# Optimization experiments

Measured on AMD Instinct MI355X. Metric: run time of the kernel, lower is better.

## Reference

```python
import jax, jax.numpy as jnp
import numpy as np

B, C, H, W = 2, 256, 64, 64
N_HEAD = 4
GROUPS = 32
EPS = 1e-5


def setup_inputs() -> dict:
    key = jax.random.key(0)
    ks = jax.random.split(key, 6)
    x = jax.random.normal(ks[0], (B, C, H, W), dtype=jnp.float32)
    # GroupNorm affine (perturbed from torch default 1/0 so grads are nontrivial)
    gn_scale = 1.0 + 0.02 * jax.random.normal(ks[1], (C,), dtype=jnp.float32)
    gn_bias = 0.02 * jax.random.normal(ks[2], (C,), dtype=jnp.float32)
    # 1x1 convs == pointwise matmuls: qkv (bias=False), out (bias=True)
    w_qkv = 0.02 * jax.random.normal(ks[3], (3 * C, C), dtype=jnp.float32)
    w_out = 0.02 * jax.random.normal(ks[4], (C, C), dtype=jnp.float32)
    b_out = 0.02 * jax.random.normal(ks[5], (C,), dtype=jnp.float32)
    return {"x": x, "gn_scale": gn_scale, "gn_bias": gn_bias,
            "w_qkv": w_qkv, "w_out": w_out, "b_out": b_out}


def _group_norm(x, scale, bias):
    b, c, h, w = x.shape
    xr = x.reshape(b, GROUPS, c // GROUPS, h, w)
    mean = jnp.mean(xr, axis=(2, 3, 4), keepdims=True)
    var = jnp.var(xr, axis=(2, 3, 4), keepdims=True)
    xr = (xr - mean) * jax.lax.rsqrt(var + EPS)
    x = xr.reshape(b, c, h, w)
    return x * scale[None, :, None, None] + bias[None, :, None, None]


def reference(x, gn_scale, gn_bias, w_qkv, w_out, b_out):
    b, c, h, w = x.shape
    head_dim = c // N_HEAD
    n = h * w
    norm = _group_norm(x, gn_scale, gn_bias)
    # 1x1 conv -> pointwise channel matmul; flatten spatial to n = h*w tokens
    qkv = jnp.einsum('oc,bcn->bon', w_qkv, norm.reshape(b, c, n))
    qkv = qkv.reshape(b, N_HEAD, 3 * head_dim, n)
    q, k, v = jnp.split(qkv, 3, axis=2)  # each [b, n_head, head_dim, n]
    # NOTE: original scales by sqrt(channel), not sqrt(head_dim)
    attn = jnp.einsum('bndq,bndk->bnqk', q, k) / jnp.sqrt(jnp.float32(c))
    attn = jax.nn.softmax(attn, axis=-1)  # [b, n_head, n, n]
    out = jnp.einsum('bnqk,bndk->bndq', attn, v)  # [b, n_head, head_dim, n]
    out = out.reshape(b, c, n)
    out = jnp.einsum('oc,bcn->bon', w_out, out) + b_out[None, :, None]
    return out.reshape(b, c, h, w) + x
```

## Files before the change

### kernel.cpp

```cpp
#include <hip/hip_runtime.h>
#include <hip/hip_bf16.h>

#define Bz 2
#define Cc 256
#define Nn 4096
#define NH 4
#define HD 64
#define NG 32
#define CPG 8
#define EPSv 1e-5f
#define NSPLIT 4
#define GNPART 4

typedef __bf16 bf16x8 __attribute__((ext_vector_type(8)));
typedef __bf16 bf16x4 __attribute__((ext_vector_type(4)));
typedef float f32x4 __attribute__((ext_vector_type(4)));
using bf16_t = __hip_bfloat16;

#define MFMA(a, b, c) __builtin_amdgcn_mfma_f32_16x16x32_bf16(a, b, c, 0, 0, 0)

#define GLOAD_LDS(g, l)                                                        \
  __builtin_amdgcn_global_load_lds(                                            \
      (const __attribute__((address_space(1))) void*)(g),                      \
      (__attribute__((address_space(3))) void*)(l), 16, 0, 0)

#define EXP2(x)                                                                \
  ({ float _r, _x = (x); asm("v_exp_f32 %0, %1" : "=v"(_r) : "v"(_x)); _r; })

__device__ __forceinline__ bf16x8 ldb8(const bf16_t* p) {
  return *reinterpret_cast<const bf16x8*>(p);
}

__global__ __launch_bounds__(256) void gn_reduce(const float* __restrict__ x,
                                                 float* __restrict__ stats4) {
  int bg = blockIdx.x;
  int part = blockIdx.y;
  const float4* p4 = reinterpret_cast<const float4*>(
      x + (size_t)bg * (CPG * Nn) + (size_t)part * (CPG * Nn / GNPART));
  float s = 0.f, ss = 0.f;
  for (int i = threadIdx.x; i < CPG * Nn / GNPART / 4; i += 256) {
    float4 v = p4[i];
    s += v.x + v.y + v.z + v.w;
    ss += v.x * v.x + v.y * v.y + v.z * v.z + v.w * v.w;
  }
#pragma unroll
  for (int off = 32; off > 0; off >>= 1) {
    s += __shfl_down(s, off);
    ss += __shfl_down(ss, off);
  }
  __shared__ float ps[4], pss[4];
  int wid = threadIdx.x >> 6;
  if ((threadIdx.x & 63) == 0) { ps[wid] = s; pss[wid] = ss; }
  __syncthreads();
  if (threadIdx.x == 0) {
    stats4[(bg * GNPART + part) * 2] = ps[0] + ps[1] + ps[2] + ps[3];
    stats4[(bg * GNPART + part) * 2 + 1] = pss[0] + pss[1] + pss[2] + pss[3];
  }
}

__global__ __launch_bounds__(256) void gn_apply(const float* __restrict__ x,
    const float* __restrict__ stats4, const float* __restrict__ sc,
    const float* __restrict__ bi, bf16_t* __restrict__ normt) {
  int b = blockIdx.z, c0 = blockIdx.y * 64, n0 = blockIdx.x * 64;
  __shared__ __align__(16) __bf16 t[64][72];
  int cx = threadIdx.x & 15, cy0 = threadIdx.x >> 4;
  const float inv = 1.f / (float)(CPG * Nn);
#pragma unroll
  for (int j = 0; j < 4; j++) {
    int c = c0 + cy0 + j * 16;
    int bg = b * NG + (c >> 3);
    float S = stats4[bg * 8] + stats4[bg * 8 + 2] + stats4[bg * 8 + 4] + stats4[bg * 8 + 6];
    float SS = stats4[bg * 8 + 1] + stats4[bg * 8 + 3] + stats4[bg * 8 + 5] + stats4[bg * 8 + 7];
    float mean = S * inv;
    float rstd = rsqrtf(SS * inv - mean * mean + EPSv);
    float a = rstd * sc[c];
    float bb = bi[c] - mean * a;
    float4 v = *reinterpret_cast<const float4*>(x + ((size_t)b * Cc + c) * Nn + n0 + cx * 4);
    bf16x4 w;
    w[0] = (__bf16)(v.x * a + bb); w[1] = (__bf16)(v.y * a + bb);
    w[2] = (__bf16)(v.z * a + bb); w[3] = (__bf16)(v.w * a + bb);
    *reinterpret_cast<bf16x4*>(&t[cy0 + j * 16][cx * 4]) = w;
  }
  __syncthreads();
  int ny = threadIdx.x >> 2, ch0 = threadIdx.x & 3;
#pragma unroll
  for (int j = 0; j < 2; j++) {
    int ch = ch0 + j * 4;
    bf16x8 o;
#pragma unroll
    for (int jj = 0; jj < 8; jj++) o[jj] = t[ch * 8 + jj][ny];
    *reinterpret_cast<bf16x8*>(normt + ((size_t)b * Nn + n0 + ny) * Cc + c0 + ch * 8) = o;
  }
}

__global__ __launch_bounds__(256) void conv_w(const float* __restrict__ wq,
    const float* __restrict__ wo, bf16_t* __restrict__ wqb,
    bf16_t* __restrict__ wob) {
  int i = blockIdx.x * 256 + threadIdx.x;
  if (i < 768 * Cc) wqb[i] = __float2bfloat16(wq[i]);
  if (i < Cc * Cc) wob[i] = __float2bfloat16(wo[i]);
}

__global__ __launch_bounds__(512) void qkv_gemm(const bf16_t* __restrict__ normt,
    const bf16_t* __restrict__ w, bf16_t* __restrict__ Qt,
    bf16_t* __restrict__ Kt, bf16_t* __restrict__ V) {
  int b = blockIdx.z;
  int h = blockIdx.y;
  int n0 = blockIdx.x * 128;
  int tid = threadIdx.x;
  int wid = tid >> 6, lane = tid & 63;
  int lr = lane & 15, lk = lane >> 4;

  __shared__ __align__(16) bf16_t wbuf[64 * 256];
  __shared__ __align__(16) __bf16 tt[128 * 80];

  const bf16_t* an = normt + ((size_t)b * Nn + n0 + wid * 16 + lr) * Cc + lk * 8;
  bf16x8 a[8];
#pragma unroll
  for (int kk = 0; kk < 8; kk++) a[kk] = ldb8(an + kk * 32);

#pragma unroll
  for (int part = 0; part < 3; part++) {
    int o0 = h * 192 + part * 64;
#pragma unroll
    for (int rnd = 0; rnd < 4; rnd++) {
      int u = rnd * 512 + tid;
      int row = u >> 5, cu = u & 31;
      int cus = (cu & 24) | ((cu & 7) ^ (row & 7));
      GLOAD_LDS(w + (size_t)(o0 + row) * Cc + cus * 8, &wbuf[u * 8]);
    }
    __syncthreads();
    f32x4 acc[4] = {};
#pragma unroll
    for (int kk = 0; kk < 8; kk++)
#pragma unroll
      for (int os = 0; os < 4; os++) {
        bf16x8 bb = ldb8(&wbuf[(os * 16 + lr) * Cc + (((kk * 4 + lk) ^ (lr & 7)) * 8)]);
        acc[os] = MFMA(a[kk], bb, acc[os]);
      }
#pragma unroll
    for (int os = 0; os < 4; os++)
#pragma unroll
      for (int r = 0; r < 4; r++)
        tt[(wid * 16 + lk * 4 + r) * 80 + os * 16 + lr] = (__bf16)acc[os][r];
    __syncthreads();
    if (part < 2) {
      bf16_t* dst = (part == 0 ? Qt : Kt) + (size_t)(b * NH + h) * Nn * HD + (size_t)n0 * HD;
      int n = tid >> 2, dch = (tid & 3) * 16;
      bf16x8 o1 = ldb8(reinterpret_cast<const bf16_t*>(&tt[n * 80 + dch]));
      bf16x8 o2 = ldb8(reinterpret_cast<const bf16_t*>(&tt[n * 80 + dch + 8]));
      *reinterpret_cast<bf16x8*>(dst + (size_t)n * HD + dch) = o1;
      *reinterpret_cast<bf16x8*>(dst + (size_t)n * HD + dch + 8) = o2;
    } else {
      bf16_t* dst = V + (size_t)(b * NH + h) * HD * Nn + n0;
      int d = tid >> 3, nch = (tid & 7) * 16;
      bf16x8 o1, o2;
#pragma unroll
      for (int j = 0; j < 8; j++) {
        o1[j] = tt[(nch + j) * 80 + d];
        o2[j] = tt[(nch + 8 + j) * 80 + d];
      }
      *reinterpret_cast<bf16x8*>(dst + (size_t)d * Nn + nch) = o1;
      *reinterpret_cast<bf16x8*>(dst + (size_t)d * Nn + nch + 8) = o2;
    }
  }
}

__global__ __launch_bounds__(256, 2) void attn_kern(const bf16_t* __restrict__ Qt,
    const bf16_t* __restrict__ Kt, const bf16_t* __restrict__ V,
    bf16_t* __restrict__ Opart, float* __restrict__ ml) {
  int z = blockIdx.z;
  int b = z & 1, sp = z >> 1;
  int h = blockIdx.y;
  int tid = threadIdx.x;
  int wid = tid >> 6, lane = tid & 63;
  int lr = lane & 15, lk = lane >> 4;
  int q0 = blockIdx.x * 256 + wid * 64;
  size_t bh = (size_t)(b * NH + h);
  const float lam = 0.0625f * 1.44269504088896f;

  const bf16_t* qp = Qt + (bh * Nn + q0 + lr) * HD + lk * 8;
  bf16x8 aqA0, aqA1, aqB0, aqB1, aqC0, aqC1, aqD0, aqD1, vone;
  {
    bf16x8 tA0 = ldb8(qp), tA1 = ldb8(qp + 32);
    bf16x8 tB0 = ldb8(qp + 16 * HD), tB1 = ldb8(qp + 16 * HD + 32);
    bf16x8 tC0 = ldb8(qp + 32 * HD), tC1 = ldb8(qp + 32 * HD + 32);
    bf16x8 tD0 = ldb8(qp + 48 * HD), tD1 = ldb8(qp + 48 * HD + 32);
#pragma unroll
    for (int j = 0; j < 8; j++) {
      aqA0[j] = (__bf16)((float)tA0[j] * lam);
      aqA1[j] = (__bf16)((float)tA1[j] * lam);
      aqB0[j] = (__bf16)((float)tB0[j] * lam);
      aqB1[j] = (__bf16)((float)tB1[j] * lam);
      aqC0[j] = (__bf16)((float)tC0[j] * lam);
      aqC1[j] = (__bf16)((float)tC1[j] * lam);
      aqD0[j] = (__bf16)((float)tD0[j] * lam);
      aqD1[j] = (__bf16)((float)tD1[j] * lam);
      vone[j] = (__bf16)1.0f;
    }
  }
  const bf16_t* kglob = Kt + bh * Nn * HD;
  const bf16_t* vglob = V + bh * HD * Nn;
  int kbeg = sp * (Nn / NSPLIT);

  __shared__ __align__(16) char lds[69632];

  int krow0 = ((wid & 1) * 64 + lane) >> 3;
  int kswz = ((lane & 7) ^ (krow0 & 7)) * 8;
  const bf16_t* ks0 = kglob + (size_t)(kbeg + krow0) * HD + kswz;
  const bf16_t* vs0 = vglob + (size_t)krow0 * Nn + kbeg + kswz;
  int kdst = (wid & 1) * 1024;

  int x0 = lr & 7;
  int aK = lr * 128 + ((lk ^ x0) * 16);
  int aK1 = aK ^ 64;
  int pwoA = 32768 + wid * 9216 + lr * 144 + lk * 8;
  int proA = 32768 + wid * 9216 + lr * 144 + lk * 16;
  int pwoB = pwoA + 2304, proB = proA + 2304;
  int pwoC = pwoA + 4608, proC = proA + 4608;
  int pwoD = pwoA + 6912, proD = proA + 6912;

  f32x4 accA[4] = {}, accB[4] = {}, accC[4] = {}, accD[4] = {};
  f32x4 l4A = {}, l4B = {}, l4C = {}, l4D = {};
  const int NT = (Nn / NSPLIT) / 64;

#define LD8(off) (*reinterpret_cast<const bf16x8*>(lds + (off)))

#define STAGE(buf, t)                                                          \
  do {                                                                         \
    if (wid < 2) {                                                             \
      GLOAD_LDS(ks0 + (size_t)(t) * 64 * HD, lds + (buf) * 8192 + kdst);       \
      GLOAD_LDS(ks0 + (size_t)(t) * 64 * HD + 16 * HD,                         \
                lds + (buf) * 8192 + kdst + 2048);                             \
      GLOAD_LDS(ks0 + (size_t)(t) * 64 * HD + 32 * HD,                         \
                lds + (buf) * 8192 + kdst + 4096);                             \
      GLOAD_LDS(ks0 + (size_t)(t) * 64 * HD + 48 * HD,                         \
                lds + (buf) * 8192 + kdst + 6144);                             \
    } else {                                                                   \
      GLOAD_LDS(vs0 + (size_t)(t) * 64, lds + 16384 + (buf) * 8192 + kdst);    \
      GLOAD_LDS(vs0 + (size_t)(t) * 64 + (size_t)16 * Nn,                      \
                lds + 16384 + (buf) * 8192 + kdst + 2048);                     \
      GLOAD_LDS(vs0 + (size_t)(t) * 64 + (size_t)32 * Nn,                      \
                lds + 16384 + (buf) * 8192 + kdst + 4096);                     \
      GLOAD_LDS(vs0 + (size_t)(t) * 64 + (size_t)48 * Nn,                      \
                lds + 16384 + (buf) * 8192 + kdst + 6144);                     \
    }                                                                          \
  } while (0)

#define QKM(m, OFF)                                                            \
  do {                                                                         \
    bf16x8 kf0 = LD8(aK + (OFF) + (m) * 2048);                                 \
    bf16x8 kf1 = LD8(aK1 + (OFF) + (m) * 2048);                                \
    sA##m = MFMA(kf0, aqA0, sA##m); sA##m = MFMA(kf1, aqA1, sA##m);            \
    sB##m = MFMA(kf0, aqB0, sB##m); sB##m = MFMA(kf1, aqB1, sB##m);            \
    sC##m = MFMA(kf0, aqC0, sC##m); sC##m = MFMA(kf1, aqC1, sC##m);            \
    sD##m = MFMA(kf0, aqD0, sD##m); sD##m = MFMA(kf1, aqD1, sD##m);            \
  } while (0)

#define PVM(m, OFF)                                                            \
  do {                                                                         \
    bf16x8 vf0 = LD8(aK + 16384 + (OFF) + (m) * 2048);                         \
    bf16x8 vf1 = LD8(aK1 + 16384 + (OFF) + (m) * 2048);                        \
    accA[m] = MFMA(vf0, paA0, accA[m]); accA[m] = MFMA(vf1, paA1, accA[m]);    \
    accB[m] = MFMA(vf0, paB0, accB[m]); accB[m] = MFMA(vf1, paB1, accB[m]);    \
    accC[m] = MFMA(vf0, paC0, accC[m]); accC[m] = MFMA(vf1, paC1, accC[m]);    \
    accD[m] = MFMA(vf0, paD0, accD[m]); accD[m] = MFMA(vf1, paD1, accD[m]);    \
  } while (0)

#define SMG(G)                                                                 \
  do {                                                                         \
    f32x4 p0, p1, p2, p3;                                                      \
    _Pragma("unroll") for (int r = 0; r < 4; r++) {                            \
      p0[r] = EXP2(s##G##0[r]); p1[r] = EXP2(s##G##1[r]);                      \
      p2[r] = EXP2(s##G##2[r]); p3[r] = EXP2(s##G##3[r]);                      \
    }                                                                          \
    bf16x4 w0, w1, w2, w3;                                                     \
    _Pragma("unroll") for (int r = 0; r < 4; r++) {                            \
      w0[r] = (__bf16)p0[r]; w1[r] = (__bf16)p1[r];                            \
      w2[r] = (__bf16)p2[r]; w3[r] = (__bf16)p3[r];                            \
    }                                                                          \
    *reinterpret_cast<bf16x4*>(lds + pwo##G) = w0;                             \
    *reinterpret_cast<bf16x4*>(lds + pwo##G + 32) = w1;                        \
    *reinterpret_cast<bf16x4*>(lds + pwo##G + 64) = w2;                        \
    *reinterpret_cast<bf16x4*>(lds + pwo##G + 96) = w3;                        \
  } while (0)

#define STEP(t, buf)                                                           \
  do {                                                                         \
    __syncthreads();                                                           \
    STAGE(buf ^ 1, (t) + 1);                                                   \
    f32x4 sA0 = {}, sA1 = {}, sA2 = {}, sA3 = {};                              \
    f32x4 sB0 = {}, sB1 = {}, sB2 = {}, sB3 = {};                              \
    f32x4 sC0 = {}, sC1 = {}, sC2 = {}, sC3 = {};                              \
    f32x4 sD0 = {}, sD1 = {}, sD2 = {}, sD3 = {};                              \
    __builtin_amdgcn_s_setprio(1);                                             \
    QKM(0, (buf) * 8192); QKM(1, (buf) * 8192);                                \
    QKM(2, (buf) * 8192); QKM(3, (buf) * 8192);                                \
    __builtin_amdgcn_s_setprio(0);                                             \
    SMG(A); SMG(B); SMG(C); SMG(D);                                            \
    bf16x8 paA0 = LD8(proA), paA1 = LD8(proA + 64);                            \
    bf16x8 paB0 = LD8(proB), paB1 = LD8(proB + 64);                            \
    bf16x8 paC0 = LD8(proC), paC1 = LD8(proC + 64);                            \
    bf16x8 paD0 = LD8(proD), paD1 = LD8(proD + 64);                            \
    __builtin_amdgcn_s_setprio(1);                                             \
    PVM(0, (buf) * 8192); PVM(1, (buf) * 8192);                                \
    PVM(2, (buf) * 8192); PVM(3, (buf) * 8192);                                \
    l4A = MFMA(vone, paA0, l4A); l4A = MFMA(vone, paA1, l4A);                  \
    l4B = MFMA(vone, paB0, l4B); l4B = MFMA(vone, paB1, l4B);                  \
    l4C = MFMA(vone, paC0, l4C); l4C = MFMA(vone, paC1, l4C);                  \
    l4D = MFMA(vone, paD0, l4D); l4D = MFMA(vone, paD1, l4D);                  \
    __builtin_amdgcn_s_setprio(0);                                             \
  } while (0)

  STAGE(0, 0);
  for (int t = 0; t < NT; t += 2) {
    STEP(t, 0);
    STEP(t + 1, 1);
  }
#undef STEP
#undef STAGE
#undef QKM
#undef PVM
#undef SMG
#undef LD8

  float invA = 1.f / l4A[0], invB = 1.f / l4B[0];
  float invC = 1.f / l4C[0], invD = 1.f / l4D[0];
  bf16_t* obA = Opart + (((size_t)z * NH + h) * Nn + q0 + lr) * HD + lk * 4;
  bf16_t* obB = obA + (size_t)16 * HD;
  bf16_t* obC = obA + (size_t)32 * HD;
  bf16_t* obD = obA + (size_t)48 * HD;
#pragma unroll
  for (int dt = 0; dt < 4; dt++) {
    bf16x4 vA, vB, vC, vD;
#pragma unroll
    for (int r = 0; r < 4; r++) {
      vA[r] = (__bf16)(accA[dt][r] * invA);
      vB[r] = (__bf16)(accB[dt][r] * invB);
      vC[r] = (__bf16)(accC[dt][r] * invC);
      vD[r] = (__bf16)(accD[dt][r] * invD);
    }
    *reinterpret_cast<bf16x4*>(obA + dt * 16) = vA;
    *reinterpret_cast<bf16x4*>(obB + dt * 16) = vB;
    *reinterpret_cast<bf16x4*>(obC + dt * 16) = vC;
    *reinterpret_cast<bf16x4*>(obD + dt * 16) = vD;
  }
  if (lk == 0) {
    size_t mb = ((size_t)z * NH + h) * Nn + q0 + lr;
    ml[mb] = l4A[0];
    ml[mb + 16] = l4B[0];
    ml[mb + 32] = l4C[0];
    ml[mb + 48] = l4D[0];
  }
}

__global__ __launch_bounds__(256) void attn_merge(const bf16_t* __restrict__ Opart,
    const float* __restrict__ ml, bf16_t* __restrict__ At) {
  int gid = blockIdx.x * 256 + threadIdx.x;
  int d0 = (gid & 7) * 8;
  int q = (gid >> 3) & (Nn - 1);
  int h = (gid >> 15) & (NH - 1);
  int b = gid >> 17;
  size_t zi[NSPLIT];
  float lv[NSPLIT];
  float L = 0.f;
#pragma unroll
  for (int s = 0; s < NSPLIT; s++) {
    zi[s] = ((size_t)(s * Bz + b) * NH + h) * Nn + q;
    lv[s] = ml[zi[s]];
    L += lv[s];
  }
  float invL = 1.f / L;
  float o[8] = {};
#pragma unroll
  for (int s = 0; s < NSPLIT; s++) {
    bf16x8 a = ldb8(Opart + zi[s] * HD + d0);
#pragma unroll
    for (int r = 0; r < 8; r++) o[r] += (float)a[r] * lv[s];
  }
  bf16x8 ov;
#pragma unroll
  for (int r = 0; r < 8; r++) ov[r] = (__bf16)(o[r] * invL);
  *reinterpret_cast<bf16x8*>(At + ((size_t)b * Nn + q) * Cc + h * HD + d0) = ov;
}

__global__ __launch_bounds__(256) void out_gemm(const bf16_t* __restrict__ At,
    const bf16_t* __restrict__ w, const float* __restrict__ bo,
    const float* __restrict__ x, float* __restrict__ out) {
  int b = blockIdx.z;
  int o0 = blockIdx.y * 64;
  int n0 = blockIdx.x * 64;
  int tid = threadIdx.x;
  int wid = tid >> 6;
  int lane = tid & 63;
  int lr = lane & 15, lk = lane >> 4;

  __shared__ __align__(16) char smem[64 * 256 * 2];
  bf16_t* wbuf = (bf16_t*)smem;
  float(*t)[68] = (float(*)[68])smem;

#pragma unroll
  for (int rnd = 0; rnd < 8; rnd++) {
    int u = rnd * 256 + tid;
    int row = u >> 5, cu = u & 31;
    int cus = (cu & 24) | ((cu & 7) ^ (row & 7));
    GLOAD_LDS(w + (size_t)(o0 + row) * Cc + cus * 8, &wbuf[u * 8]);
  }
  const bf16_t* aa = At + ((size_t)b * Nn + n0 + wid * 16 + lr) * Cc + lk * 8;
  f32x4 acc[4] = {};
  __syncthreads();
#pragma unroll
  for (int kk = 0; kk < Cc / 32; kk++) {
    bf16x8 a = ldb8(aa + kk * 32);
#pragma unroll
    for (int os = 0; os < 4; os++) {
      bf16x8 bb = ldb8(&wbuf[(os * 16 + lr) * Cc + (((kk * 4 + lk) ^ (lr & 7)) * 8)]);
      acc[os] = MFMA(a, bb, acc[os]);
    }
  }
  __syncthreads();
#pragma unroll
  for (int os = 0; os < 4; os++)
#pragma unroll
    for (int r = 0; r < 4; r++)
      t[wid * 16 + lk * 4 + r][os * 16 + lr] = acc[os][r];
  __syncthreads();
  int orow = tid >> 2;
  int nch = (tid & 3) * 16;
  size_t base = ((size_t)b * Cc + o0 + orow) * Nn + n0 + nch;
  float bv = bo[o0 + orow];
#pragma unroll
  for (int j = 0; j < 16; j++)
    out[base + j] = t[nch + j][orow] + bv + x[base + j];
}

extern "C" void kernel_launch(void* const* d_in, const int* in_sizes, int n_in,
                              void* d_out, int out_size, void* d_ws, size_t ws_size,
                              hipStream_t stream) {
  const float* x = (const float*)d_in[0];
  const float* gn_scale = (const float*)d_in[1];
  const float* gn_bias = (const float*)d_in[2];
  const float* w_qkv = (const float*)d_in[3];
  const float* w_out = (const float*)d_in[4];
  const float* b_out = (const float*)d_in[5];
  float* out = (float*)d_out;
  char* ws = (char*)d_ws;

  float* stats4 = (float*)(ws + 0);
  bf16_t* wout_b = (bf16_t*)(ws + 4096);
  bf16_t* Qt = (bf16_t*)(ws + 139264);
  bf16_t* At = (bf16_t*)(ws + 139264);
  bf16_t* Kt = (bf16_t*)(ws + 4333568);
  bf16_t* V = (bf16_t*)(ws + 8527872);
  bf16_t* wqkv_b = (bf16_t*)(ws + 12722176);
  bf16_t* normt = (bf16_t*)(ws + 13115392);
  bf16_t* Opart = (bf16_t*)(ws + 12722176);
  float* ml = (float*)(ws + 29499392);

  conv_w<<<768, 256, 0, stream>>>(w_qkv, w_out, wqkv_b, wout_b);
  gn_reduce<<<dim3(Bz * NG, GNPART), 256, 0, stream>>>(x, stats4);
  gn_apply<<<dim3(Nn / 64, Cc / 64, Bz), 256, 0, stream>>>(x, stats4, gn_scale, gn_bias, normt);
  qkv_gemm<<<dim3(Nn / 128, NH, Bz), 512, 0, stream>>>(normt, wqkv_b, Qt, Kt, V);
  attn_kern<<<dim3(Nn / 256, NH, Bz * NSPLIT), 256, 0, stream>>>(Qt, Kt, V, Opart, ml);
  attn_merge<<<Bz * NH * Nn * HD / 8 / 256, 256, 0, stream>>>(Opart, ml, At);
  out_gemm<<<dim3(Nn / 64, Cc / 64, Bz), 256, 0, stream>>>(At, wout_b, b_out, x, out);
}
```

Measured before the change: 82.11 us.

## Fuse split-attention merge into output GEMM and merge prep kernels

Combines weight bf16 conversion and groupnorm partial reduction into one launch using block-index partitioning. Removes the separate attention merge kernel by having each output-GEMM block combine the split partial outputs for its 64 rows into LDS before the MFMA loop. This drops two launches and the intermediate At buffer roundtrip, at the cost of recomputing the merge once per output-channel block and raising shared memory use to about 65KB per block.

```diff
diff --git a/kernel.cpp b/kernel.cpp
--- a/kernel.cpp
+++ b/kernel.cpp
@@ -31,30 +31,39 @@
   return *reinterpret_cast<const bf16x8*>(p);
 }
 
-__global__ __launch_bounds__(256) void gn_reduce(const float* __restrict__ x,
-                                                 float* __restrict__ stats4) {
-  int bg = blockIdx.x;
-  int part = blockIdx.y;
-  const float4* p4 = reinterpret_cast<const float4*>(
-      x + (size_t)bg * (CPG * Nn) + (size_t)part * (CPG * Nn / GNPART));
-  float s = 0.f, ss = 0.f;
-  for (int i = threadIdx.x; i < CPG * Nn / GNPART / 4; i += 256) {
-    float4 v = p4[i];
-    s += v.x + v.y + v.z + v.w;
-    ss += v.x * v.x + v.y * v.y + v.z * v.z + v.w * v.w;
-  }
-#pragma unroll
-  for (int off = 32; off > 0; off >>= 1) {
-    s += __shfl_down(s, off);
-    ss += __shfl_down(ss, off);
-  }
-  __shared__ float ps[4], pss[4];
-  int wid = threadIdx.x >> 6;
-  if ((threadIdx.x & 63) == 0) { ps[wid] = s; pss[wid] = ss; }
-  __syncthreads();
-  if (threadIdx.x == 0) {
-    stats4[(bg * GNPART + part) * 2] = ps[0] + ps[1] + ps[2] + ps[3];
-    stats4[(bg * GNPART + part) * 2 + 1] = pss[0] + pss[1] + pss[2] + pss[3];
+__global__ __launch_bounds__(256) void prep_kern(const float* __restrict__ wq,
+    const float* __restrict__ wo, bf16_t* __restrict__ wqb,
+    bf16_t* __restrict__ wob, const float* __restrict__ x,
+    float* __restrict__ stats4) {
+  int bid = blockIdx.x;
+  if (bid < 768) {
+    int i = bid * 256 + threadIdx.x;
+    if (i < 768 * Cc) wqb[i] = __float2bfloat16(wq[i]);
+    if (i < Cc * Cc) wob[i] = __float2bfloat16(wo[i]);
+  } else {
+    int idx = bid - 768;
+    int bg = idx >> 2, part = idx & 3;
+    const float4* p4 = reinterpret_cast<const float4*>(
+        x + (size_t)bg * (CPG * Nn) + (size_t)part * (CPG * Nn / GNPART));
+    float s = 0.f, ss = 0.f;
+    for (int i = threadIdx.x; i < CPG * Nn / GNPART / 4; i += 256) {
+      float4 v = p4[i];
+      s += v.x + v.y + v.z + v.w;
+      ss += v.x * v.x + v.y * v.y + v.z * v.z + v.w * v.w;
+    }
+#pragma unroll
+    for (int off = 32; off > 0; off >>= 1) {
+      s += __shfl_down(s, off);
+      ss += __shfl_down(ss, off);
+    }
+    __shared__ float ps[4], pss[4];
+    int wid = threadIdx.x >> 6;
+    if ((threadIdx.x & 63) == 0) { ps[wid] = s; pss[wid] = ss; }
+    __syncthreads();
+    if (threadIdx.x == 0) {
+      stats4[(bg * GNPART + part) * 2] = ps[0] + ps[1] + ps[2] + ps[3];
+      stats4[(bg * GNPART + part) * 2 + 1] = pss[0] + pss[1] + pss[2] + pss[3];
+    }
   }
 }
 
@@ -91,14 +100,6 @@
     for (int jj = 0; jj < 8; jj++) o[jj] = t[ch * 8 + jj][ny];
     *reinterpret_cast<bf16x8*>(normt + ((size_t)b * Nn + n0 + ny) * Cc + c0 + ch * 8) = o;
   }
-}
-
-__global__ __launch_bounds__(256) void conv_w(const float* __restrict__ wq,
-    const float* __restrict__ wo, bf16_t* __restrict__ wqb,
-    bf16_t* __restrict__ wob) {
-  int i = blockIdx.x * 256 + threadIdx.x;
-  if (i < 768 * Cc) wqb[i] = __float2bfloat16(wq[i]);
-  if (i < Cc * Cc) wob[i] = __float2bfloat16(wo[i]);
 }
 
 __global__ __launch_bounds__(512) void qkv_gemm(const bf16_t* __restrict__ normt,
@@ -354,39 +355,10 @@
   }
 }
 
-__global__ __launch_bounds__(256) void attn_merge(const bf16_t* __restrict__ Opart,
-    const float* __restrict__ ml, bf16_t* __restrict__ At) {
-  int gid = blockIdx.x * 256 + threadIdx.x;
-  int d0 = (gid & 7) * 8;
-  int q = (gid >> 3) & (Nn - 1);
-  int h = (gid >> 15) & (NH - 1);
-  int b = gid >> 17;
-  size_t zi[NSPLIT];
-  float lv[NSPLIT];
-  float L = 0.f;
-#pragma unroll
-  for (int s = 0; s < NSPLIT; s++) {
-    zi[s] = ((size_t)(s * Bz + b) * NH + h) * Nn + q;
-    lv[s] = ml[zi[s]];
-    L += lv[s];
-  }
-  float invL = 1.f / L;
-  float o[8] = {};
-#pragma unroll
-  for (int s = 0; s < NSPLIT; s++) {
-    bf16x8 a = ldb8(Opart + zi[s] * HD + d0);
-#pragma unroll
-    for (int r = 0; r < 8; r++) o[r] += (float)a[r] * lv[s];
-  }
-  bf16x8 ov;
-#pragma unroll
-  for (int r = 0; r < 8; r++) ov[r] = (__bf16)(o[r] * invL);
-  *reinterpret_cast<bf16x8*>(At + ((size_t)b * Nn + q) * Cc + h * HD + d0) = ov;
-}
-
-__global__ __launch_bounds__(256) void out_gemm(const bf16_t* __restrict__ At,
-    const bf16_t* __restrict__ w, const float* __restrict__ bo,
-    const float* __restrict__ x, float* __restrict__ out) {
+__global__ __launch_bounds__(256) void out_gemm(const bf16_t* __restrict__ Opart,
+    const float* __restrict__ ml, const bf16_t* __restrict__ w,
+    const float* __restrict__ bo, const float* __restrict__ x,
+    float* __restrict__ out) {
   int b = blockIdx.z;
   int o0 = blockIdx.y * 64;
   int n0 = blockIdx.x * 64;
@@ -395,9 +367,10 @@
   int lane = tid & 63;
   int lr = lane & 15, lk = lane >> 4;
 
-  __shared__ __align__(16) char smem[64 * 256 * 2];
+  __shared__ __align__(16) char smem[66560];
   bf16_t* wbuf = (bf16_t*)smem;
   float(*t)[68] = (float(*)[68])smem;
+  char* att = smem + 32768;
 
 #pragma unroll
   for (int rnd = 0; rnd < 8; rnd++) {
@@ -406,12 +379,42 @@
     int cus = (cu & 24) | ((cu & 7) ^ (row & 7));
     GLOAD_LDS(w + (size_t)(o0 + row) * Cc + cus * 8, &wbuf[u * 8]);
   }
-  const bf16_t* aa = At + ((size_t)b * Nn + n0 + wid * 16 + lr) * Cc + lk * 8;
+  {
+    int h = wid, row = lane;
+    const size_t sstr = (size_t)Bz * NH * Nn * HD;
+    float lv[NSPLIT];
+    float L = 0.f;
+#pragma unroll
+    for (int s = 0; s < NSPLIT; s++) {
+      lv[s] = ml[((size_t)(s * Bz + b) * NH + h) * Nn + n0 + row];
+      L += lv[s];
+    }
+    float invL = 1.f / L;
+#pragma unroll
+    for (int s = 0; s < NSPLIT; s++) lv[s] *= invL;
+    const bf16_t* op0 = Opart + (((size_t)b * NH + h) * Nn + n0 + row) * HD;
+    char* arow = att + row * 528 + h * 128;
+#pragma unroll
+    for (int j8 = 0; j8 < 8; j8++) {
+      float o[8] = {};
+#pragma unroll
+      for (int s = 0; s < NSPLIT; s++) {
+        bf16x8 a = ldb8(op0 + s * sstr + j8 * 8);
+#pragma unroll
+        for (int r = 0; r < 8; r++) o[r] += (float)a[r] * lv[s];
+      }
+      bf16x8 ov;
+#pragma unroll
+      for (int r = 0; r < 8; r++) ov[r] = (__bf16)o[r];
+      *reinterpret_cast<bf16x8*>(arow + j8 * 16) = ov;
+    }
+  }
   f32x4 acc[4] = {};
   __syncthreads();
 #pragma unroll
   for (int kk = 0; kk < Cc / 32; kk++) {
-    bf16x8 a = ldb8(aa + kk * 32);
+    bf16x8 a = *reinterpret_cast<const bf16x8*>(
+        att + (wid * 16 + lr) * 528 + kk * 64 + lk * 16);
 #pragma unroll
     for (int os = 0; os < 4; os++) {
       bf16x8 bb = ldb8(&wbuf[(os * 16 + lr) * Cc + (((kk * 4 + lk) ^ (lr & 7)) * 8)]);
@@ -449,7 +452,6 @@
   float* stats4 = (float*)(ws + 0);
   bf16_t* wout_b = (bf16_t*)(ws + 4096);
   bf16_t* Qt = (bf16_t*)(ws + 139264);
-  bf16_t* At = (bf16_t*)(ws + 139264);
   bf16_t* Kt = (bf16_t*)(ws + 4333568);
   bf16_t* V = (bf16_t*)(ws + 8527872);
   bf16_t* wqkv_b = (bf16_t*)(ws + 12722176);
@@ -457,11 +459,9 @@
   bf16_t* Opart = (bf16_t*)(ws + 12722176);
   float* ml = (float*)(ws + 29499392);
 
-  conv_w<<<768, 256, 0, stream>>>(w_qkv, w_out, wqkv_b, wout_b);
-  gn_reduce<<<dim3(Bz * NG, GNPART), 256, 0, stream>>>(x, stats4);
+  prep_kern<<<1024, 256, 0, stream>>>(w_qkv, w_out, wqkv_b, wout_b, x, stats4);
   gn_apply<<<dim3(Nn / 64, Cc / 64, Bz), 256, 0, stream>>>(x, stats4, gn_scale, gn_bias, normt);
   qkv_gemm<<<dim3(Nn / 128, NH, Bz), 512, 0, stream>>>(normt, wqkv_b, Qt, Kt, V);
   attn_kern<<<dim3(Nn / 256, NH, Bz * NSPLIT), 256, 0, stream>>>(Qt, Kt, V, Opart, ml);
-  attn_merge<<<Bz * NH * Nn * HD / 8 / 256, 256, 0, stream>>>(Opart, ml, At);
-  out_gemm<<<dim3(Nn / 64, Cc / 64, Bz), 256, 0, stream>>>(At, wout_b, b_out, x, out);
-}
+  out_gemm<<<dim3(Nn / 64, Cc / 64, Bz), 256, 0, stream>>>(Opart, ml, wout_b, b_out, x, out);
+}
```

New measurement: 87.82 us. 6.9% more time.
